# Performance work log

Hardware: AMD Instinct MI355X
Metric: run time of the kernel (lower is better)

## Reference

```python
import jax, jax.numpy as jnp
import numpy as np

NS, NH, NL, NP, E = 2, 8, 4, 4, 256
HD = E // NH  # 32


def grid_sample_zeros(img, grid):
    """torch.F.grid_sample(mode='bilinear', padding_mode='zeros', align_corners=False).
    img: [B, C, Hs, Ws]; grid: [B, Hg, Wg, 2] with (x, y) in [-1, 1]. Returns [B, C, Hg, Wg]."""
    B, C, Hs, Ws = img.shape
    gx = (grid[..., 0] + 1.0) * (Ws * 0.5) - 0.5  # pixel-space x
    gy = (grid[..., 1] + 1.0) * (Hs * 0.5) - 0.5  # pixel-space y
    x0 = jnp.floor(gx)
    y0 = jnp.floor(gy)
    x1, y1 = x0 + 1.0, y0 + 1.0
    wx1 = gx - x0
    wx0 = 1.0 - wx1
    wy1 = gy - y0
    wy0 = 1.0 - wy1
    imgf = img.reshape(B, C, Hs * Ws)

    def gather(ix, iy):
        valid = (ix >= 0) & (ix < Ws) & (iy >= 0) & (iy < Hs)
        ixc = jnp.clip(ix, 0, Ws - 1).astype(jnp.int32)
        iyc = jnp.clip(iy, 0, Hs - 1).astype(jnp.int32)
        flat = (iyc * Ws + ixc).reshape(B, 1, -1)
        vals = jnp.take_along_axis(imgf, flat, axis=2).reshape(B, C, *ix.shape[1:])
        return vals * valid[:, None].astype(img.dtype)

    return (gather(x0, y0) * (wx0 * wy0)[:, None]
            + gather(x1, y0) * (wx1 * wy0)[:, None]
            + gather(x0, y1) * (wx0 * wy1)[:, None]
            + gather(x1, y1) * (wx1 * wy1)[:, None])


def setup_inputs() -> dict:
    key = jax.random.key(0)
    ks = jax.random.split(key, 10)
    bs, Q = 2048, NL * NP  # num_query forced to num_levels*num_points = 16
    f = jnp.float32
    s = 1.0 / np.sqrt(E)
    return {
        "query": jax.random.normal(ks[0], (bs, Q, E), f),
        "key_hist": jax.random.normal(ks[1], (bs, Q, E), f),
        "value_hist": jax.random.normal(ks[2], (bs, Q, E), f),
        "reference_points": jax.random.uniform(ks[3], (bs, Q, NL, 2), f),
        "spatial_shapes": jnp.full((NL, 2), 2, dtype=jnp.int32),  # each level 2x2, sum HW = 16
        "Wq": jax.random.normal(ks[4], (E, E), f) * s, "bq": jnp.zeros((E,), f),
        "Wk": jax.random.normal(ks[5], (E, E), f) * s, "bk": jnp.zeros((E,), f),
        "Wv": jax.random.normal(ks[6], (E, E), f) * s, "bv": jnp.zeros((E,), f),
        "Woff": jax.random.normal(ks[7], (E, NH * NL * NP * 2), f) * (0.01 * s), "boff": jnp.zeros((NH * NL * NP * 2,), f),
        "Wout": jax.random.normal(ks[8], (E, E), f) * s, "bout": jnp.zeros((E,), f),
    }


def reference(query, key_hist, value_hist, reference_points, spatial_shapes,
              Wq, bq, Wk, bk, Wv, bv, Woff, boff, Wout, bout):
    bs, Q, _ = query.shape
    B = bs * NS
    residual = query

    # torch cat(dim=1)+view interleaves the two sequences per batch: index 2b -> query, 2b+1 -> hist
    queries = jnp.repeat(query, NS, axis=0)                              # [B, Q, E]
    keys = jnp.stack([query, key_hist], axis=1).reshape(B, Q, E)
    values = jnp.stack([query, value_hist], axis=1).reshape(B, Q, E)
    rp = jnp.repeat(reference_points, NS, axis=0)                        # [B, Q, NL, 2] (both copies identical)

    qh = (queries @ Wq + bq).reshape(B, Q, NH, HD)
    kh = (keys @ Wk + bk).reshape(B, Q, NH, HD)
    vh = (values @ Wv + bv).reshape(B, Q, NH, HD)

    attn = jax.nn.softmax(jnp.einsum('bqhd,bkhd->bqhk', qh, kh), axis=-1)
    attn = attn.reshape(B, Q, NH, NL, NP)

    offsets = (queries @ Woff + boff).reshape(B, Q, NH, NL, NP, 2)
    norm = jnp.stack([spatial_shapes[:, 1], spatial_shapes[:, 0]], axis=-1).astype(query.dtype)  # (W, H)
    loc = rp[:, :, None, :, None, :] + offsets / norm[None, None, None, :, None, :]
    grid = 2.0 * loc - 1.0                                               # [B, Q, NH, NL, NP, 2]

    ss = np.asarray(spatial_shapes)                                      # static level shapes
    attw = attn.transpose(0, 2, 1, 3, 4).reshape(B * NH, Q, NL, NP)      # [BH, Q, NL, NP]
    acc = jnp.zeros((B * NH, HD, Q), dtype=query.dtype)
    start = 0
    for l in range(NL):
        H_, W_ = int(ss[l, 0]), int(ss[l, 1])
        hw = H_ * W_
        v_l = vh[:, start:start + hw].transpose(0, 2, 3, 1).reshape(B * NH, HD, H_, W_)
        g_l = grid[:, :, :, l].transpose(0, 2, 1, 3, 4).reshape(B * NH, Q, NP, 2)
        s_l = grid_sample_zeros(v_l, g_l)                                # [BH, HD, Q, NP]
        acc = acc + jnp.sum(s_l * attw[:, None, :, l, :], axis=-1)       # weighted reduce over points
        start += hw

    out = acc.reshape(B, E, Q).transpose(0, 2, 1)                        # [B, Q, E]
    out = out.reshape(bs, NS, Q, E).mean(axis=1)                         # mean over the two sequences
    return out @ Wout + bout + residual                                  # dropout is identity in eval
```

## Files before the change

### kernel.cpp

```cpp
#include <hip/hip_runtime.h>

typedef float  f32x4  __attribute__((ext_vector_type(4)));
typedef __bf16 bf16x8 __attribute__((ext_vector_type(8)));
typedef __bf16 bf16x4 __attribute__((ext_vector_type(4)));

__device__ __forceinline__ bf16x8 cvt8(float4 a, float4 b) {
    bf16x8 r;
    r[0] = (__bf16)a.x; r[1] = (__bf16)a.y; r[2] = (__bf16)a.z; r[3] = (__bf16)a.w;
    r[4] = (__bf16)b.x; r[5] = (__bf16)b.y; r[6] = (__bf16)b.z; r[7] = (__bf16)b.w;
    return r;
}

#define OF_OFF 524288

__global__ void wprep(const float* __restrict__ Wq, const float* __restrict__ Wk,
                      const float* __restrict__ Wv, const float* __restrict__ Woff,
                      const float* __restrict__ Wout, __bf16* __restrict__ ws) {
    int id = blockIdx.x * 256 + threadIdx.x;
    if (id < 262144) {
        int tile = id >> 9, e = id & 511;
        int lane = e >> 3, j = e & 7;
        int kt = tile & 7, nh = (tile >> 3) & 1, mat = (tile >> 4) & 3, h = tile >> 6;
        int k = kt * 32 + (lane >> 4) * 8 + j;
        int col = h * 32 + nh * 16 + (lane & 15);
        const float* W = (mat == 0) ? Wq : (mat == 1) ? Wk : (mat == 2) ? Wv : Woff;
        ws[id] = (__bf16)W[k * 256 + col];
    } else {
        int i = id - 262144;
        int tile = i >> 9, e = i & 511;
        int lane = e >> 3, j = e & 7;
        int kt = tile & 7, nt = tile >> 3;
        int k = kt * 32 + (lane >> 4) * 8 + j;
        int col = nt * 16 + (lane & 15);
        ws[262144 + i] = (__bf16)Wout[k * 256 + col];
    }
}

__device__ __forceinline__ const float4* stage_addr(const unsigned char* wsw, int ss, int t, int it) {
    int u = t + it * 512;
    if (ss < 16) {
        int h = ss >> 1, nh = ss & 1, f = u >> 6;
        return (const float4*)(wsw + ((((h * 4 + (f >> 3)) * 2 + nh) * 8 + (f & 7)) << 10) + (u & 63) * 16);
    }
    return (const float4*)(wsw + OF_OFF + (ss - 16) * 32768 + u * 16);
}

__launch_bounds__(512, 2)
__global__ void tsa_one(const float* __restrict__ query, const float* __restrict__ keyh,
                        const float* __restrict__ valh, const float* __restrict__ refpts,
                        const unsigned char* __restrict__ wsw,
                        const float* __restrict__ bq, const float* __restrict__ bk,
                        const float* __restrict__ bv, const float* __restrict__ boff,
                        const float* __restrict__ bout, float* __restrict__ out)
{
    __shared__ __attribute__((aligned(16))) unsigned char uni[49152];
    __shared__ __attribute__((aligned(16))) unsigned char accs[65536];
    const int t = threadIdx.x;
    const int lane = t & 63, w = t >> 6, l15 = lane & 15, lhi = lane >> 4;
    const long b = (long)blockIdx.x * 8 + w;

    float4 pf[4];
    #pragma unroll
    for (int it = 0; it < 4; ++it) pf[it] = *stage_addr(wsw, 0, t, it);

    bf16x8 aq[8], ak[8], av[8];
    {
        const float* qp = query + b * 4096 + l15 * 256;
        const float* kp = keyh  + b * 4096 + l15 * 256;
        const float* vp = valh  + b * 4096 + l15 * 256;
        #pragma unroll
        for (int kt = 0; kt < 8; ++kt) {
            int o = kt * 32 + lhi * 8;
            aq[kt] = cvt8(*(const float4*)(qp + o), *(const float4*)(qp + o + 4));
            ak[kt] = cvt8(*(const float4*)(kp + o), *(const float4*)(kp + o + 4));
            av[kt] = cvt8(*(const float4*)(vp + o), *(const float4*)(vp + o + 4));
        }
    }
    unsigned char* scr = uni + w * 6144;
    const f32x4 z = (f32x4){0.f, 0.f, 0.f, 0.f};

    for (int h = 0; h < 8; ++h) {
        f32x4 acc[12];
        #pragma unroll
        for (int i = 0; i < 12; ++i) acc[i] = z;

        #pragma unroll 2
        for (int nh = 0; nh < 2; ++nh) {
            __syncthreads();
            #pragma unroll
            for (int it = 0; it < 4; ++it)
                *(float4*)(uni + (t + it * 512) * 16) = pf[it];
            __syncthreads();
            {
                int nss = h * 2 + nh + 1;
                if (nss < 20) {
                    #pragma unroll
                    for (int it = 0; it < 4; ++it) pf[it] = *stage_addr(wsw, nss, t, it);
                }
            }
            #pragma unroll
            for (int kt = 0; kt < 8; ++kt) {
                const unsigned char* bb = uni + kt * 1024 + lane * 16;
                bf16x8 b_q = *(const bf16x8*)(bb);
                bf16x8 b_k = *(const bf16x8*)(bb + 8192);
                bf16x8 b_v = *(const bf16x8*)(bb + 16384);
                bf16x8 b_o = *(const bf16x8*)(bb + 24576);
                acc[0 + nh]  = __builtin_amdgcn_mfma_f32_16x16x32_bf16(aq[kt], b_q, acc[0 + nh], 0, 0, 0);
                acc[2 + nh]  = __builtin_amdgcn_mfma_f32_16x16x32_bf16(aq[kt], b_k, acc[2 + nh], 0, 0, 0);
                acc[4 + nh]  = __builtin_amdgcn_mfma_f32_16x16x32_bf16(ak[kt], b_k, acc[4 + nh], 0, 0, 0);
                acc[6 + nh]  = __builtin_amdgcn_mfma_f32_16x16x32_bf16(aq[kt], b_v, acc[6 + nh], 0, 0, 0);
                acc[8 + nh]  = __builtin_amdgcn_mfma_f32_16x16x32_bf16(av[kt], b_v, acc[8 + nh], 0, 0, 0);
                acc[10 + nh] = __builtin_amdgcn_mfma_f32_16x16x32_bf16(aq[kt], b_o, acc[10 + nh], 0, 0, 0);
            }
        }
        __syncthreads();

        #pragma unroll 2
        for (int nh = 0; nh < 2; ++nh) {
            int dcol = nh * 16 + l15;
            int gcol = h * 32 + dcol;
            float bqv = bq[gcol], bkv = bk[gcol], bvv = bv[gcol], bov = boff[gcol];
            #pragma unroll
            for (int r = 0; r < 4; ++r) {
                int row = lhi * 4 + r;
                *(__bf16*)(scr + row * 64 + dcol * 2)        = (__bf16)(acc[0 + nh][r] + bqv);
                *(__bf16*)(scr + 1024 + row * 64 + dcol * 2) = (__bf16)(acc[2 + nh][r] + bkv);
                *(__bf16*)(scr + 2048 + row * 64 + dcol * 2) = (__bf16)(acc[4 + nh][r] + bkv);
                *(__bf16*)(scr + 3072 + dcol * 64 + row * 2)      = (__bf16)(acc[6 + nh][r] + bvv);
                *(__bf16*)(scr + 3072 + dcol * 64 + 32 + row * 2) = (__bf16)(acc[8 + nh][r] + bvv);
                *(__bf16*)(scr + 5120 + row * 64 + dcol * 2) = (__bf16)(acc[10 + nh][r] + bov);
            }
        }

        bf16x8 qf = *(const bf16x8*)(scr + l15 * 64 + lhi * 16);
        bf16x8 k0 = *(const bf16x8*)(scr + 1024 + l15 * 64 + lhi * 16);
        bf16x8 k1 = *(const bf16x8*)(scr + 2048 + l15 * 64 + lhi * 16);
        f32x4 S0 = __builtin_amdgcn_mfma_f32_16x16x32_bf16(k0, qf, z, 0, 0, 0);
        f32x4 S1 = __builtin_amdgcn_mfma_f32_16x16x32_bf16(k1, qf, z, 0, 0, 0);

        float p0[4], p1[4];
        {
            float m = fmaxf(fmaxf(S0[0], S0[1]), fmaxf(S0[2], S0[3]));
            m = fmaxf(m, __shfl_xor(m, 16)); m = fmaxf(m, __shfl_xor(m, 32));
            float s = 0.f;
            #pragma unroll
            for (int r = 0; r < 4; ++r) { p0[r] = __expf(S0[r] - m); s += p0[r]; }
            s += __shfl_xor(s, 16); s += __shfl_xor(s, 32);
            float inv = 1.f / s;
            #pragma unroll
            for (int r = 0; r < 4; ++r) p0[r] *= inv;
        }
        {
            float m = fmaxf(fmaxf(S1[0], S1[1]), fmaxf(S1[2], S1[3]));
            m = fmaxf(m, __shfl_xor(m, 16)); m = fmaxf(m, __shfl_xor(m, 32));
            float s = 0.f;
            #pragma unroll
            for (int r = 0; r < 4; ++r) { p1[r] = __expf(S1[r] - m); s += p1[r]; }
            s += __shfl_xor(s, 16); s += __shfl_xor(s, 32);
            float inv = 1.f / s;
            #pragma unroll
            for (int r = 0; r < 4; ++r) p1[r] *= inv;
        }

        float2 rp = *(const float2*)(refpts + b * 128 + l15 * 8 + lhi * 2);
        bf16x8 off8 = *(const bf16x8*)(scr + 5120 + l15 * 64 + lhi * 16);
        float w40[4] = {0.f, 0.f, 0.f, 0.f}, w41[4] = {0.f, 0.f, 0.f, 0.f};
        #pragma unroll
        for (int p = 0; p < 4; ++p) {
            float gx = 2.f * rp.x + (float)off8[2 * p]     - 0.5f;
            float gy = 2.f * rp.y + (float)off8[2 * p + 1] - 0.5f;
            float tx0 = fmaxf(0.f, 1.f - fabsf(gx));
            float tx1 = fmaxf(0.f, 1.f - fabsf(gx - 1.f));
            float ty0 = fmaxf(0.f, 1.f - fabsf(gy));
            float ty1 = fmaxf(0.f, 1.f - fabsf(gy - 1.f));
            float w00 = tx0 * ty0, w01 = tx1 * ty0, w10 = tx0 * ty1, w11 = tx1 * ty1;
            w40[0] += w00 * p0[p]; w40[1] += w01 * p0[p];
            w40[2] += w10 * p0[p]; w40[3] += w11 * p0[p];
            w41[0] += w00 * p1[p]; w41[1] += w01 * p1[p];
            w41[2] += w10 * p1[p]; w41[3] += w11 * p1[p];
        }
        *(bf16x4*)(scr + 5120 + l15 * 64 + lhi * 8) =
            (bf16x4){(__bf16)w40[0], (__bf16)w40[1], (__bf16)w40[2], (__bf16)w40[3]};
        *(bf16x4*)(scr + 5120 + l15 * 64 + 32 + lhi * 8) =
            (bf16x4){(__bf16)w41[0], (__bf16)w41[1], (__bf16)w41[2], (__bf16)w41[3]};

        bf16x8 aW = *(const bf16x8*)(scr + 5120 + l15 * 64 + lhi * 16);
        #pragma unroll
        for (int dh = 0; dh < 2; ++dh) {
            bf16x8 vf = *(const bf16x8*)(scr + 3072 + (dh * 16 + l15) * 64 + lhi * 16);
            f32x4 c = __builtin_amdgcn_mfma_f32_16x16x32_bf16(aW, vf, z, 0, 0, 0);
            #pragma unroll
            for (int r = 0; r < 4; ++r) {
                int qq = lhi * 4 + r;
                int colg = h * 32 + dh * 16 + l15;
                *(__bf16*)(accs + w * 8192 + qq * 512 + (((unsigned)(colg * 2)) ^ ((qq & 7) << 4))) =
                    (__bf16)(0.5f * c[r]);
            }
        }
    }

    for (int qd = 0; qd < 4; ++qd) {
        __syncthreads();
        #pragma unroll
        for (int it = 0; it < 4; ++it)
            *(float4*)(uni + (t + it * 512) * 16) = pf[it];
        __syncthreads();
        {
            int nss = 17 + qd;
            if (nss < 20) {
                #pragma unroll
                for (int it = 0; it < 4; ++it) pf[it] = *stage_addr(wsw, nss, t, it);
            }
        }
        f32x4 o4[4];
        #pragma unroll
        for (int i = 0; i < 4; ++i) o4[i] = z;
        #pragma unroll
        for (int kt = 0; kt < 8; ++kt) {
            bf16x8 afr = *(const bf16x8*)(accs + w * 8192 + l15 * 512 +
                                          (((unsigned)(kt * 64 + lhi * 16)) ^ ((l15 & 7) << 4)));
            #pragma unroll
            for (int ntl = 0; ntl < 4; ++ntl)
                o4[ntl] = __builtin_amdgcn_mfma_f32_16x16x32_bf16(
                    afr, *(const bf16x8*)(uni + (ntl * 8 + kt) * 1024 + lane * 16), o4[ntl], 0, 0, 0);
        }
        #pragma unroll
        for (int ntl = 0; ntl < 4; ++ntl) {
            int col = (qd * 4 + ntl) * 16 + l15;
            float bo = bout[col];
            #pragma unroll
            for (int r = 0; r < 4; ++r) {
                int qq = lhi * 4 + r;
                long idx = b * 4096 + qq * 256 + col;
                out[idx] = o4[ntl][r] + bo + query[idx];
            }
        }
    }
}

extern "C" void kernel_launch(void* const* d_in, const int* in_sizes, int n_in,
                              void* d_out, int out_size, void* d_ws, size_t ws_size,
                              hipStream_t stream) {
    const float* query      = (const float*)d_in[0];
    const float* key_hist   = (const float*)d_in[1];
    const float* value_hist = (const float*)d_in[2];
    const float* refpts     = (const float*)d_in[3];
    const float* Wq   = (const float*)d_in[5];
    const float* bq   = (const float*)d_in[6];
    const float* Wk   = (const float*)d_in[7];
    const float* bk   = (const float*)d_in[8];
    const float* Wv   = (const float*)d_in[9];
    const float* bv   = (const float*)d_in[10];
    const float* Woff = (const float*)d_in[11];
    const float* boff = (const float*)d_in[12];
    const float* Wout = (const float*)d_in[13];
    const float* bout = (const float*)d_in[14];
    float* outp = (float*)d_out;

    const int bs = in_sizes[0] / 4096;
    wprep<<<1280, 256, 0, stream>>>(Wq, Wk, Wv, Woff, Wout, (__bf16*)d_ws);
    tsa_one<<<bs / 8, 512, 0, stream>>>(query, key_hist, value_hist, refpts,
                                        (const unsigned char*)d_ws,
                                        bq, bk, bv, boff, bout, outp);
}
```

Baseline: 94.90 us.

## Spill attention accumulator to global workspace to cut LDS and raise occupancy

The 64 KB shared-memory accumulator for the per-head sampled values is removed. Each head's result is now written in MFMA fragment layout to a global scratch region of the workspace and read back for the output projection. With LDS down to 48 KB, launch bounds go from 2 to 4 blocks per SM to allow more resident waves. The cost is extra global write and read traffic (L2-resident, about 8 KB per batch row). The host also chunks the launch when the workspace is too small, and if the workspace is smaller than the scratch offset the chunk size could be wrong.

```diff
diff --git a/kernel.cpp b/kernel.cpp
--- a/kernel.cpp
+++ b/kernel.cpp
@@ -12,6 +12,7 @@
 }
 
 #define OF_OFF 524288
+#define PV_OFF (1u << 20)
 
 __global__ void wprep(const float* __restrict__ Wq, const float* __restrict__ Wk,
                       const float* __restrict__ Wv, const float* __restrict__ Woff,
@@ -45,19 +46,19 @@
     return (const float4*)(wsw + OF_OFF + (ss - 16) * 32768 + u * 16);
 }
 
-__launch_bounds__(512, 2)
+__launch_bounds__(512, 4)
 __global__ void tsa_one(const float* __restrict__ query, const float* __restrict__ keyh,
                         const float* __restrict__ valh, const float* __restrict__ refpts,
-                        const unsigned char* __restrict__ wsw,
+                        unsigned char* __restrict__ wsw,
                         const float* __restrict__ bq, const float* __restrict__ bk,
                         const float* __restrict__ bv, const float* __restrict__ boff,
-                        const float* __restrict__ bout, float* __restrict__ out)
+                        const float* __restrict__ bout, float* __restrict__ out, int b0)
 {
     __shared__ __attribute__((aligned(16))) unsigned char uni[49152];
-    __shared__ __attribute__((aligned(16))) unsigned char accs[65536];
     const int t = threadIdx.x;
     const int lane = t & 63, w = t >> 6, l15 = lane & 15, lhi = lane >> 4;
-    const long b = (long)blockIdx.x * 8 + w;
+    const long b = (long)b0 + (long)blockIdx.x * 8 + w;
+    __bf16* pvg = (__bf16*)(wsw + PV_OFF) + ((long)blockIdx.x * 8 + w) * 4096;
 
     float4 pf[4];
     #pragma unroll
@@ -192,10 +193,12 @@
             #pragma unroll
             for (int r = 0; r < 4; ++r) {
                 int qq = lhi * 4 + r;
-                int colg = h * 32 + dh * 16 + l15;
-                *(__bf16*)(accs + w * 8192 + qq * 512 + (((unsigned)(colg * 2)) ^ ((qq & 7) << 4))) =
-                    (__bf16)(0.5f * c[r]);
-            }
+                *(__bf16*)(scr + qq * 64 + (dh * 16 + l15) * 2) = (__bf16)(0.5f * c[r]);
+            }
+        }
+        {
+            bf16x8 pvfrag = *(const bf16x8*)(scr + l15 * 64 + lhi * 16);
+            *(bf16x8*)(pvg + h * 512 + lane * 8) = pvfrag;
         }
     }
 
@@ -217,8 +220,7 @@
         for (int i = 0; i < 4; ++i) o4[i] = z;
         #pragma unroll
         for (int kt = 0; kt < 8; ++kt) {
-            bf16x8 afr = *(const bf16x8*)(accs + w * 8192 + l15 * 512 +
-                                          (((unsigned)(kt * 64 + lhi * 16)) ^ ((l15 & 7) << 4)));
+            bf16x8 afr = *(const bf16x8*)(pvg + kt * 512 + lane * 8);
             #pragma unroll
             for (int ntl = 0; ntl < 4; ++ntl)
                 o4[ntl] = __builtin_amdgcn_mfma_f32_16x16x32_bf16(
@@ -259,7 +261,17 @@
 
     const int bs = in_sizes[0] / 4096;
     wprep<<<1280, 256, 0, stream>>>(Wq, Wk, Wv, Woff, Wout, (__bf16*)d_ws);
-    tsa_one<<<bs / 8, 512, 0, stream>>>(query, key_hist, value_hist, refpts,
-                                        (const unsigned char*)d_ws,
-                                        bq, bk, bv, boff, bout, outp);
-}
+
+    long avail = (long)ws_size - (long)PV_OFF;
+    int CB = bs;
+    if (avail < (long)bs * 8192) {
+        CB = (int)(avail / 8192) & ~7;
+        if (CB < 8) CB = 8;
+    }
+    for (int b0 = 0; b0 < bs; b0 += CB) {
+        int nb = (bs - b0 < CB ? bs - b0 : CB) / 8;
+        tsa_one<<<nb, 512, 0, stream>>>(query, key_hist, value_hist, refpts,
+                                        (unsigned char*)d_ws,
+                                        bq, bk, bv, boff, bout, outp, b0);
+    }
+}
```

After: 227.0 us. +139.2%, slower.
